# Optimization experiments

Measured on AMD Instinct MI355X. Metric: run time of the kernel, lower is better.

## Reference

```python
import jax, jax.numpy as jnp
import numpy as np

N = 20000      # num nodes
E = 320000     # num edges
F_IN = 512
HEADS = 8
D = 64         # out_features per head (512 / 8)
ALPHA = 0.2    # leaky relu slope
EPS = 1e-16


def setup_inputs() -> dict:
    key = jax.random.key(0)
    k1, k2, k3, k4, k5 = jax.random.split(key, 5)
    x = jax.random.normal(k1, (N, F_IN), dtype=jnp.float32)
    edge_index = jax.random.randint(k2, (2, E), 0, N, dtype=jnp.int64)
    # per-head parameters (xavier-normal-ish scale)
    s_w = np.sqrt(2.0 / (F_IN + D))
    W_e = jax.random.normal(k3, (HEADS, F_IN, D), dtype=jnp.float32) * s_w
    W_r = jax.random.normal(k4, (HEADS, F_IN, D), dtype=jnp.float32) * s_w
    # attention vector over concat of [h_src, h_dst, diff, |diff|, prod] -> 5*D
    s_a = np.sqrt(2.0 / (1 + 5 * D))
    a = jax.random.normal(k5, (HEADS, 5 * D), dtype=jnp.float32) * s_a
    return {"x": x, "edge_index": edge_index, "W_e": W_e, "W_r": W_r, "a": a}


def _gat_forward(x, edge_index, W_e, W_r, a):
    src = edge_index[0]  # [E] softmax / output rows
    dst = edge_index[1]  # [E]

    h_e = jnp.einsum('nf,hfd->hnd', x, W_e)  # [H,N,D]
    h_r = jnp.einsum('nf,hfd->hnd', x, W_r)  # [H,N,D]

    a_src, a_dst, a_dif, a_abs, a_prd = jnp.split(a, 5, axis=1)  # each [H,D]

    # node-level dot products for the linear concat parts, then gather
    s_src = jnp.einsum('hnd,hd->hn', h_e, a_src)[:, src]  # [H,E]
    s_dst = jnp.einsum('hnd,hd->hn', h_e, a_dst)[:, dst]  # [H,E]

    hr_src = h_r[:, src]            # [H,E,D]
    hr_dst = h_r[:, dst]            # [H,E,D]
    diff = hr_dst - hr_src          # [H,E,D]
    score = (s_src + s_dst
             + jnp.einsum('hed,hd->he', diff, a_dif)
             + jnp.einsum('hed,hd->he', jnp.abs(diff), a_abs)
             + jnp.einsum('hed,hd->he', hr_src * hr_dst, a_prd))  # [H,E]

    alpha = jax.nn.leaky_relu(score, negative_slope=ALPHA)  # [H,E]

    # sparse softmax over edges grouped by source node
    alpha_t = alpha.T  # [E,H]
    m = jax.ops.segment_max(alpha_t, src, num_segments=N)        # [N,H]
    ex = jnp.exp(alpha_t - m[src])                                # [E,H]
    denom = jax.ops.segment_sum(ex, src, num_segments=N)[src]    # [E,H]
    att = ex / (denom + EPS)                                      # [E,H]

    # spmm: out[src] += att * h_e[dst]
    msg = att[:, :, None] * jnp.transpose(h_e[:, dst], (1, 0, 2))  # [E,H,D]
    out = jax.ops.segment_sum(msg, src, num_segments=N)            # [N,H,D]
    return out.reshape(N, HEADS * D)  # concat heads along feature dim


def reference(x, edge_index, W_e, W_r, a):
    return _gat_forward(x, edge_index, W_e, W_r, a)
```

## Files before the change

### kernel.cpp

```cpp
#include <hip/hip_runtime.h>
#include <hip/hip_bf16.h>

#define N_NODES 20000
#define N_EDGES 320000
#define F_IN 512
#define HEADS 8
#define DH 64

typedef __attribute__((ext_vector_type(8))) short short8;
typedef __attribute__((ext_vector_type(4))) float f32x4;

__device__ inline short f2bf(float f) {
  __hip_bfloat16 h = __float2bfloat16(f);
  return __builtin_bit_cast(short, h);
}
__device__ inline void unpack8(short8 s, float f[8]) {
  uint4 u = __builtin_bit_cast(uint4, s);
  f[0] = __builtin_bit_cast(float, u.x << 16);
  f[1] = __builtin_bit_cast(float, u.x & 0xFFFF0000u);
  f[2] = __builtin_bit_cast(float, u.y << 16);
  f[3] = __builtin_bit_cast(float, u.y & 0xFFFF0000u);
  f[4] = __builtin_bit_cast(float, u.z << 16);
  f[5] = __builtin_bit_cast(float, u.z & 0xFFFF0000u);
  f[6] = __builtin_bit_cast(float, u.w << 16);
  f[7] = __builtin_bit_cast(float, u.w & 0xFFFF0000u);
}
__device__ __forceinline__ void async_copy16(void* lds_base, const void* g) {
  __builtin_amdgcn_global_load_lds(
      (const __attribute__((address_space(1))) unsigned int*)g,
      (__attribute__((address_space(3))) unsigned int*)lds_base, 16, 0, 0);
}

__global__ __launch_bounds__(256) void cast_x_kernel(
    const float* __restrict__ x, short* __restrict__ xb)
{
  int i = (blockIdx.x * 256 + threadIdx.x) * 4;
  if (i < N_NODES * F_IN) {
    float4 v = *(const float4*)&x[i];
    short4 o;
    o.x = f2bf(v.x); o.y = f2bf(v.y); o.z = f2bf(v.z); o.w = f2bf(v.w);
    *(short4*)&xb[i] = o;
  }
}

__global__ __launch_bounds__(256) void cast_w_kernel(
    const float* __restrict__ We, const float* __restrict__ Wr, short* __restrict__ Wt)
{
  __shared__ short tile[64 * 65];
  const int b = blockIdx.x;
  const int kt = (b & 7) * 64;
  const int h = (b >> 3) & 7;
  const int mat = b >> 6;
  const float* __restrict__ W = (mat ? Wr : We) + (size_t)h * F_IN * DH;
  #pragma unroll
  for (int r = 0; r < 16; ++r) {
    int idx = r * 256 + threadIdx.x;
    int k = idx >> 6, d = idx & 63;
    tile[d * 65 + k] = f2bf(W[(size_t)(kt + k) * DH + d]);
  }
  __syncthreads();
  short* __restrict__ Wo = Wt + (size_t)(mat * 8 + h) * 64 * F_IN;
  #pragma unroll
  for (int r = 0; r < 16; ++r) {
    int idx = r * 256 + threadIdx.x;
    int d = idx >> 6, k = idx & 63;
    Wo[(size_t)d * F_IN + kt + k] = tile[d * 65 + k];
  }
}

#define GBM 128
#define GBN 128
#define GBK 64

__global__ __launch_bounds__(256) void gemm_mfma(
    const short* __restrict__ xb, const short* __restrict__ Wt,
    short* __restrict__ he, short* __restrict__ hr,
    const float* __restrict__ a,
    float* __restrict__ ssrc, float* __restrict__ sdst)
{
  __shared__ short As[GBM * GBK];
  __shared__ short Bs[GBN * GBK];
  const int tid = threadIdx.x;
  const int m0 = blockIdx.x * GBM;
  const int n0 = blockIdx.y * GBN;
  const int wv = tid >> 6, lane = tid & 63, quad = lane >> 4, l16 = lane & 15;
  const int wm = (wv >> 1) * 64;
  const int wn = (wv & 1) * 64;
  const int lrow = lane >> 3;
  const int gc = (lane & 7) ^ (lrow & 7);

  f32x4 acc[4][4] = {};

  for (int kt = 0; kt < F_IN; kt += GBK) {
    #pragma unroll
    for (int s = 0; s < 4; ++s) {
      int seg = wv * 4 + s;
      int row = seg * 8 + lrow;
      async_copy16(&As[seg * 512],
                   &xb[(size_t)(m0 + row) * F_IN + kt + gc * 8]);
      async_copy16(&Bs[seg * 512],
                   &Wt[(size_t)(n0 + row) * F_IN + kt + gc * 8]);
    }
    __syncthreads();
    #pragma unroll
    for (int ks = 0; ks < 2; ++ks) {
      short8 af[4], bf4[4];
      const int ch = ((ks << 2) + quad) ^ (l16 & 7);
      #pragma unroll
      for (int i = 0; i < 4; ++i)
        af[i] = *(const short8*)&As[(wm + i * 16 + l16) * GBK + ch * 8];
      #pragma unroll
      for (int j = 0; j < 4; ++j)
        bf4[j] = *(const short8*)&Bs[(wn + j * 16 + l16) * GBK + ch * 8];
      #pragma unroll
      for (int i = 0; i < 4; ++i)
        #pragma unroll
        for (int j = 0; j < 4; ++j)
          acc[i][j] = __builtin_amdgcn_mfma_f32_16x16x32_bf16(af[i], bf4[j], acc[i][j], 0, 0, 0);
    }
    __syncthreads();
  }

  const int cb = blockIdx.y * 2 + (wv & 1);
  const int mat = cb >> 3, h = cb & 7;
  short* __restrict__ C = mat ? hr : he;
  #pragma unroll
  for (int i = 0; i < 4; ++i) {
    #pragma unroll
    for (int r = 0; r < 4; ++r) {
      int m = m0 + wm + i * 16 + quad * 4 + r;
      if (m < N_NODES) {
        #pragma unroll
        for (int j = 0; j < 4; ++j)
          C[((size_t)m * HEADS + h) * DH + j * 16 + l16] = f2bf(acc[i][j][r]);
      }
    }
  }

  if (mat == 0) {
    float as4[4], ad4[4];
    #pragma unroll
    for (int j = 0; j < 4; ++j) {
      as4[j] = a[h * 320 + j * 16 + l16];
      ad4[j] = a[h * 320 + 64 + j * 16 + l16];
    }
    #pragma unroll
    for (int i = 0; i < 4; ++i) {
      #pragma unroll
      for (int r = 0; r < 4; ++r) {
        int m = m0 + wm + i * 16 + quad * 4 + r;
        float v1 = 0.f, v2 = 0.f;
        #pragma unroll
        for (int j = 0; j < 4; ++j) {
          v1 = fmaf(acc[i][j][r], as4[j], v1);
          v2 = fmaf(acc[i][j][r], ad4[j], v2);
        }
        #pragma unroll
        for (int s = 1; s < 16; s <<= 1) {
          v1 += __shfl_xor(v1, s);
          v2 += __shfl_xor(v2, s);
        }
        if (l16 == 0 && m < N_NODES) {
          ssrc[(size_t)m * HEADS + h] = v1;
          sdst[(size_t)m * HEADS + h] = v2;
        }
      }
    }
  }
}

__global__ void hist_kernel(const int* __restrict__ ei, int* __restrict__ deg) {
  int e = blockIdx.x * blockDim.x + threadIdx.x;
  if (e < N_EDGES) atomicAdd(&deg[ei[e]], 1);
}

#define SC_NB 20

__global__ __launch_bounds__(1024) void scan_pre(
    const int* __restrict__ deg, int* __restrict__ bsum)
{
  __shared__ int wsum[16];
  int tid = threadIdx.x, wv = tid >> 6, ln = tid & 63;
  int i = blockIdx.x * 1024 + tid;
  int v = (i < N_NODES) ? deg[i] : 0;
  #pragma unroll
  for (int d = 32; d >= 1; d >>= 1) v += __shfl_xor(v, d);
  if (ln == 0) wsum[wv] = v;
  __syncthreads();
  if (tid == 0) {
    int s = 0;
    #pragma unroll
    for (int k = 0; k < 16; ++k) s += wsum[k];
    bsum[blockIdx.x] = s;
  }
}

__global__ void scan_mid(const int* __restrict__ bsum, int* __restrict__ bbase,
                         int* __restrict__ off)
{
  int ln = threadIdx.x;
  int v = (ln < SC_NB) ? bsum[ln] : 0;
  int s = v;
  #pragma unroll
  for (int d = 1; d < 64; d <<= 1) {
    int t = __shfl_up(s, d);
    if (ln >= d) s += t;
  }
  if (ln < SC_NB) bbase[ln] = s - v;
  if (ln == SC_NB - 1) off[N_NODES] = s;
}

__global__ __launch_bounds__(1024) void scan_fin(
    const int* __restrict__ deg, const int* __restrict__ bbase, int* __restrict__ off)
{
  __shared__ int wsum[16];
  int tid = threadIdx.x, wv = tid >> 6, ln = tid & 63;
  int i = blockIdx.x * 1024 + tid;
  int v = (i < N_NODES) ? deg[i] : 0;
  int s = v;
  #pragma unroll
  for (int d = 1; d < 64; d <<= 1) {
    int t = __shfl_up(s, d);
    if (ln >= d) s += t;
  }
  if (ln == 63) wsum[wv] = s;
  __syncthreads();
  if (wv == 0 && ln < 16) {
    int t = wsum[ln];
    #pragma unroll
    for (int d = 1; d < 16; d <<= 1) {
      int u = __shfl_up(t, d);
      if (ln >= d) t += u;
    }
    wsum[ln] = t;
  }
  __syncthreads();
  int base = bbase[blockIdx.x] + (wv ? wsum[wv - 1] : 0);
  if (i < N_NODES) off[i] = base + s - v;
}

__global__ void scatter_kernel(const int* __restrict__ ei, const int* __restrict__ off,
                               int* __restrict__ cnt, int* __restrict__ csr_dst) {
  int e = blockIdx.x * blockDim.x + threadIdx.x;
  if (e < N_EDGES) {
    int s = ei[e];
    int t = ei[N_EDGES + e];
    int pos = off[s] + atomicAdd(&cnt[s], 1);
    csr_dst[pos] = t;
  }
}

#define ATTN_BLOCKS 1024
#define ATTN_WAVES (ATTN_BLOCKS * 8)

__global__ __launch_bounds__(512) void attn_kernel(
    const short* __restrict__ he, const short* __restrict__ hr,
    const float* __restrict__ a, const float* __restrict__ ssrc,
    const float* __restrict__ sdst, const int* __restrict__ off,
    const int* __restrict__ csr_dst, float* __restrict__ out)
{
  const int lane = threadIdx.x & 63;
  const int h = lane >> 3;
  const int d0 = (lane & 7) * 8;
  const int ab = h * 320;
  float adif[8], aabs[8], aprd[8];
  *(float4*)&adif[0] = *(const float4*)&a[ab + 128 + d0];
  *(float4*)&adif[4] = *(const float4*)&a[ab + 128 + d0 + 4];
  *(float4*)&aabs[0] = *(const float4*)&a[ab + 192 + d0];
  *(float4*)&aabs[4] = *(const float4*)&a[ab + 192 + d0 + 4];
  *(float4*)&aprd[0] = *(const float4*)&a[ab + 256 + d0];
  *(float4*)&aprd[4] = *(const float4*)&a[ab + 256 + d0 + 4];

  const int gw0 = blockIdx.x * 8 + (threadIdx.x >> 6);

  for (int n = gw0; n < N_NODES; n += ATTN_WAVES) {
    const int beg = off[n], end = off[n + 1];
    float hrn[8];
    unpack8(*(const short8*)&hr[(size_t)n * 512 + lane * 8], hrn);
    const float sbase = ssrc[(size_t)n * HEADS + h];
    float denom = 0.f;
    float acc[8] = {};

    auto edge = [&](short8 hr8, short8 he8, float sd) {
      float hrd[8], hed[8];
      unpack8(hr8, hrd);
      unpack8(he8, hed);
      float v = 0.f;
      #pragma unroll
      for (int j = 0; j < 8; ++j) {
        float df = hrd[j] - hrn[j];
        v = fmaf(df, adif[j], v);
        v = fmaf(fabsf(df), aabs[j], v);
        v = fmaf(hrn[j] * hrd[j], aprd[j], v);
      }
      v += __shfl_xor(v, 1);
      v += __shfl_xor(v, 2);
      v += __shfl_xor(v, 4);
      float sc = sbase + sd + v;
      sc = fmaxf(sc, 0.2f * sc);
      float ex = __expf(sc);
      denom += ex;
      #pragma unroll
      for (int j = 0; j < 8; ++j) acc[j] = fmaf(ex, hed[j], acc[j]);
    };

    int i = beg;
    for (; i + 4 <= end; i += 4) {
      int t0 = csr_dst[i], t1 = csr_dst[i + 1], t2 = csr_dst[i + 2], t3 = csr_dst[i + 3];
      short8 r0 = *(const short8*)&hr[(size_t)t0 * 512 + lane * 8];
      short8 e0 = *(const short8*)&he[(size_t)t0 * 512 + lane * 8];
      short8 r1 = *(const short8*)&hr[(size_t)t1 * 512 + lane * 8];
      short8 e1 = *(const short8*)&he[(size_t)t1 * 512 + lane * 8];
      short8 r2 = *(const short8*)&hr[(size_t)t2 * 512 + lane * 8];
      short8 e2 = *(const short8*)&he[(size_t)t2 * 512 + lane * 8];
      short8 r3 = *(const short8*)&hr[(size_t)t3 * 512 + lane * 8];
      short8 e3 = *(const short8*)&he[(size_t)t3 * 512 + lane * 8];
      float s0 = sdst[(size_t)t0 * HEADS + h];
      float s1 = sdst[(size_t)t1 * HEADS + h];
      float s2 = sdst[(size_t)t2 * HEADS + h];
      float s3 = sdst[(size_t)t3 * HEADS + h];
      edge(r0, e0, s0);
      edge(r1, e1, s1);
      edge(r2, e2, s2);
      edge(r3, e3, s3);
    }
    for (; i < end; ++i) {
      int t = csr_dst[i];
      short8 r0 = *(const short8*)&hr[(size_t)t * 512 + lane * 8];
      short8 e0 = *(const short8*)&he[(size_t)t * 512 + lane * 8];
      float s0 = sdst[(size_t)t * HEADS + h];
      edge(r0, e0, s0);
    }

    float inv = 1.f / (denom + 1e-16f);
    float4 o0, o1;
    o0.x = acc[0] * inv; o0.y = acc[1] * inv; o0.z = acc[2] * inv; o0.w = acc[3] * inv;
    o1.x = acc[4] * inv; o1.y = acc[5] * inv; o1.z = acc[6] * inv; o1.w = acc[7] * inv;
    *(float4*)&out[(size_t)n * 512 + lane * 8] = o0;
    *(float4*)&out[(size_t)n * 512 + lane * 8 + 4] = o1;
  }
}

extern "C" void kernel_launch(void* const* d_in, const int* in_sizes, int n_in,
                              void* d_out, int out_size, void* d_ws, size_t ws_size,
                              hipStream_t stream) {
  const float* x  = (const float*)d_in[0];
  const int*   ei = (const int*)d_in[1];
  const float* We = (const float*)d_in[2];
  const float* Wr = (const float*)d_in[3];
  const float* a  = (const float*)d_in[4];
  float* out = (float*)d_out;

  char* ws = (char*)d_ws;
  size_t p = 0;
  auto alloc = [&](size_t bytes) {
    void* r = ws + p;
    p = (p + bytes + 255) & ~(size_t)255;
    return r;
  };
  short* xb = (short*)alloc(sizeof(short) * (size_t)N_NODES * F_IN);
  short* Wt = (short*)alloc(sizeof(short) * 2 * HEADS * F_IN * DH);
  short* he = (short*)alloc(sizeof(short) * (size_t)N_NODES * HEADS * DH);
  short* hr = (short*)alloc(sizeof(short) * (size_t)N_NODES * HEADS * DH);
  float* ssrc = (float*)alloc(sizeof(float) * (size_t)N_NODES * HEADS);
  float* sdst = (float*)alloc(sizeof(float) * (size_t)N_NODES * HEADS);
  int* degcnt = (int*)alloc(sizeof(int) * 2 * N_NODES);
  int* deg = degcnt;
  int* cnt = degcnt + N_NODES;
  int* off = (int*)alloc(sizeof(int) * (N_NODES + 1));
  int* csr = (int*)alloc(sizeof(int) * N_EDGES);
  int* bsum = (int*)alloc(sizeof(int) * SC_NB);
  int* bbase = (int*)alloc(sizeof(int) * SC_NB);

  hipMemsetAsync(degcnt, 0, sizeof(int) * 2 * N_NODES, stream);

  cast_x_kernel<<<(N_NODES * F_IN / 4 + 255) / 256, 256, 0, stream>>>(x, xb);
  cast_w_kernel<<<128, 256, 0, stream>>>(We, Wr, Wt);

  dim3 g1((N_NODES + GBM - 1) / GBM, 8);
  gemm_mfma<<<g1, 256, 0, stream>>>(xb, Wt, he, hr, a, ssrc, sdst);

  hist_kernel<<<(N_EDGES + 255) / 256, 256, 0, stream>>>(ei, deg);
  scan_pre<<<SC_NB, 1024, 0, stream>>>(deg, bsum);
  scan_mid<<<1, 64, 0, stream>>>(bsum, bbase, off);
  scan_fin<<<SC_NB, 1024, 0, stream>>>(deg, bbase, off);
  scatter_kernel<<<(N_EDGES + 255) / 256, 256, 0, stream>>>(ei, off, cnt, csr);
  attn_kernel<<<ATTN_BLOCKS, 512, 0, stream>>>(he, hr, a, ssrc, sdst, off, csr, out);
}
```

Measured before the change: 281.0 us.

## Remap GEMM blocks per XCD and launch one wave per node in attention

Result: faster. 274.4 us (-2.3%).

```diff
diff --git a/kernel.cpp b/kernel.cpp
--- a/kernel.cpp
+++ b/kernel.cpp
@@ -71,6 +71,8 @@
 #define GBM 128
 #define GBN 128
 #define GBK 64
+#define MT_TOTAL 157
+#define MT_PER_GRP 20
 
 __global__ __launch_bounds__(256) void gemm_mfma(
     const short* __restrict__ xb, const short* __restrict__ Wt,
@@ -78,11 +80,18 @@
     const float* __restrict__ a,
     float* __restrict__ ssrc, float* __restrict__ sdst)
 {
+  const int b = blockIdx.x;
+  const int g = b & 7;
+  const int j = b >> 3;
+  const int m_tile = g * MT_PER_GRP + (j >> 3);
+  const int c_tile = j & 7;
+  if (m_tile >= MT_TOTAL) return;
+
   __shared__ short As[GBM * GBK];
   __shared__ short Bs[GBN * GBK];
   const int tid = threadIdx.x;
-  const int m0 = blockIdx.x * GBM;
-  const int n0 = blockIdx.y * GBN;
+  const int m0 = m_tile * GBM;
+  const int n0 = c_tile * GBN;
   const int wv = tid >> 6, lane = tid & 63, quad = lane >> 4, l16 = lane & 15;
   const int wm = (wv >> 1) * 64;
   const int wn = (wv & 1) * 64;
@@ -110,18 +119,18 @@
       for (int i = 0; i < 4; ++i)
         af[i] = *(const short8*)&As[(wm + i * 16 + l16) * GBK + ch * 8];
       #pragma unroll
-      for (int j = 0; j < 4; ++j)
-        bf4[j] = *(const short8*)&Bs[(wn + j * 16 + l16) * GBK + ch * 8];
+      for (int jj = 0; jj < 4; ++jj)
+        bf4[jj] = *(const short8*)&Bs[(wn + jj * 16 + l16) * GBK + ch * 8];
       #pragma unroll
       for (int i = 0; i < 4; ++i)
         #pragma unroll
-        for (int j = 0; j < 4; ++j)
-          acc[i][j] = __builtin_amdgcn_mfma_f32_16x16x32_bf16(af[i], bf4[j], acc[i][j], 0, 0, 0);
+        for (int jj = 0; jj < 4; ++jj)
+          acc[i][jj] = __builtin_amdgcn_mfma_f32_16x16x32_bf16(af[i], bf4[jj], acc[i][jj], 0, 0, 0);
     }
     __syncthreads();
   }
 
-  const int cb = blockIdx.y * 2 + (wv & 1);
+  const int cb = c_tile * 2 + (wv & 1);
   const int mat = cb >> 3, h = cb & 7;
   short* __restrict__ C = mat ? hr : he;
   #pragma unroll
@@ -131,8 +140,8 @@
       int m = m0 + wm + i * 16 + quad * 4 + r;
       if (m < N_NODES) {
         #pragma unroll
-        for (int j = 0; j < 4; ++j)
-          C[((size_t)m * HEADS + h) * DH + j * 16 + l16] = f2bf(acc[i][j][r]);
+        for (int jj = 0; jj < 4; ++jj)
+          C[((size_t)m * HEADS + h) * DH + jj * 16 + l16] = f2bf(acc[i][jj][r]);
       }
     }
   }
@@ -140,9 +149,9 @@
   if (mat == 0) {
     float as4[4], ad4[4];
     #pragma unroll
-    for (int j = 0; j < 4; ++j) {
-      as4[j] = a[h * 320 + j * 16 + l16];
-      ad4[j] = a[h * 320 + 64 + j * 16 + l16];
+    for (int jj = 0; jj < 4; ++jj) {
+      as4[jj] = a[h * 320 + jj * 16 + l16];
+      ad4[jj] = a[h * 320 + 64 + jj * 16 + l16];
     }
     #pragma unroll
     for (int i = 0; i < 4; ++i) {
@@ -151,9 +160,9 @@
         int m = m0 + wm + i * 16 + quad * 4 + r;
         float v1 = 0.f, v2 = 0.f;
         #pragma unroll
-        for (int j = 0; j < 4; ++j) {
-          v1 = fmaf(acc[i][j][r], as4[j], v1);
-          v2 = fmaf(acc[i][j][r], ad4[j], v2);
+        for (int jj = 0; jj < 4; ++jj) {
+          v1 = fmaf(acc[i][jj][r], as4[jj], v1);
+          v2 = fmaf(acc[i][jj][r], ad4[jj], v2);
         }
         #pragma unroll
         for (int s = 1; s < 16; s <<= 1) {
@@ -250,95 +259,74 @@
   }
 }
 
-#define ATTN_BLOCKS 1024
-#define ATTN_WAVES (ATTN_BLOCKS * 8)
-
-__global__ __launch_bounds__(512) void attn_kernel(
+__global__ __launch_bounds__(256) void attn_kernel(
     const short* __restrict__ he, const short* __restrict__ hr,
     const float* __restrict__ a, const float* __restrict__ ssrc,
     const float* __restrict__ sdst, const int* __restrict__ off,
     const int* __restrict__ csr_dst, float* __restrict__ out)
 {
+  const int wv = threadIdx.x >> 6;
+  const int n = blockIdx.x * 4 + wv;
   const int lane = threadIdx.x & 63;
   const int h = lane >> 3;
   const int d0 = (lane & 7) * 8;
+  const int beg = off[n], end = off[n + 1];
+
+  float hrn[8];
+  unpack8(*(const short8*)&hr[(size_t)n * 512 + lane * 8], hrn);
+  float adif[8], aabs[8], aprd[8];
   const int ab = h * 320;
-  float adif[8], aabs[8], aprd[8];
   *(float4*)&adif[0] = *(const float4*)&a[ab + 128 + d0];
   *(float4*)&adif[4] = *(const float4*)&a[ab + 128 + d0 + 4];
   *(float4*)&aabs[0] = *(const float4*)&a[ab + 192 + d0];
   *(float4*)&aabs[4] = *(const float4*)&a[ab + 192 + d0 + 4];
   *(float4*)&aprd[0] = *(const float4*)&a[ab + 256 + d0];
   *(float4*)&aprd[4] = *(const float4*)&a[ab + 256 + d0 + 4];
-
-  const int gw0 = blockIdx.x * 8 + (threadIdx.x >> 6);
-
-  for (int n = gw0; n < N_NODES; n += ATTN_WAVES) {
-    const int beg = off[n], end = off[n + 1];
-    float hrn[8];
-    unpack8(*(const short8*)&hr[(size_t)n * 512 + lane * 8], hrn);
-    const float sbase = ssrc[(size_t)n * HEADS + h];
-    float denom = 0.f;
-    float acc[8] = {};
-
-    auto edge = [&](short8 hr8, short8 he8, float sd) {
-      float hrd[8], hed[8];
-      unpack8(hr8, hrd);
-      unpack8(he8, hed);
-      float v = 0.f;
-      #pragma unroll
-      for (int j = 0; j < 8; ++j) {
-        float df = hrd[j] - hrn[j];
-        v = fmaf(df, adif[j], v);
-        v = fmaf(fabsf(df), aabs[j], v);
-        v = fmaf(hrn[j] * hrd[j], aprd[j], v);
-      }
-      v += __shfl_xor(v, 1);
-      v += __shfl_xor(v, 2);
-      v += __shfl_xor(v, 4);
-      float sc = sbase + sd + v;
-      sc = fmaxf(sc, 0.2f * sc);
-      float ex = __expf(sc);
-      denom += ex;
-      #pragma unroll
-      for (int j = 0; j < 8; ++j) acc[j] = fmaf(ex, hed[j], acc[j]);
-    };
-
-    int i = beg;
-    for (; i + 4 <= end; i += 4) {
-      int t0 = csr_dst[i], t1 = csr_dst[i + 1], t2 = csr_dst[i + 2], t3 = csr_dst[i + 3];
-      short8 r0 = *(const short8*)&hr[(size_t)t0 * 512 + lane * 8];
-      short8 e0 = *(const short8*)&he[(size_t)t0 * 512 + lane * 8];
-      short8 r1 = *(const short8*)&hr[(size_t)t1 * 512 + lane * 8];
-      short8 e1 = *(const short8*)&he[(size_t)t1 * 512 + lane * 8];
-      short8 r2 = *(const short8*)&hr[(size_t)t2 * 512 + lane * 8];
-      short8 e2 = *(const short8*)&he[(size_t)t2 * 512 + lane * 8];
-      short8 r3 = *(const short8*)&hr[(size_t)t3 * 512 + lane * 8];
-      short8 e3 = *(const short8*)&he[(size_t)t3 * 512 + lane * 8];
-      float s0 = sdst[(size_t)t0 * HEADS + h];
-      float s1 = sdst[(size_t)t1 * HEADS + h];
-      float s2 = sdst[(size_t)t2 * HEADS + h];
-      float s3 = sdst[(size_t)t3 * HEADS + h];
-      edge(r0, e0, s0);
-      edge(r1, e1, s1);
-      edge(r2, e2, s2);
-      edge(r3, e3, s3);
-    }
-    for (; i < end; ++i) {
-      int t = csr_dst[i];
-      short8 r0 = *(const short8*)&hr[(size_t)t * 512 + lane * 8];
-      short8 e0 = *(const short8*)&he[(size_t)t * 512 + lane * 8];
-      float s0 = sdst[(size_t)t * HEADS + h];
-      edge(r0, e0, s0);
-    }
-
-    float inv = 1.f / (denom + 1e-16f);
-    float4 o0, o1;
-    o0.x = acc[0] * inv; o0.y = acc[1] * inv; o0.z = acc[2] * inv; o0.w = acc[3] * inv;
-    o1.x = acc[4] * inv; o1.y = acc[5] * inv; o1.z = acc[6] * inv; o1.w = acc[7] * inv;
-    *(float4*)&out[(size_t)n * 512 + lane * 8] = o0;
-    *(float4*)&out[(size_t)n * 512 + lane * 8 + 4] = o1;
-  }
+  const float sbase = ssrc[(size_t)n * HEADS + h];
+
+  float denom = 0.f;
+  float acc[8] = {};
+
+  auto process = [&](int t) {
+    short8 hr8 = *(const short8*)&hr[(size_t)t * 512 + lane * 8];
+    short8 he8 = *(const short8*)&he[(size_t)t * 512 + lane * 8];
+    float sd = sdst[(size_t)t * HEADS + h];
+    float hrd[8], hed[8];
+    unpack8(hr8, hrd);
+    unpack8(he8, hed);
+    float v = 0.f;
+    #pragma unroll
+    for (int j = 0; j < 8; ++j) {
+      float df = hrd[j] - hrn[j];
+      v = fmaf(df, adif[j], v);
+      v = fmaf(fabsf(df), aabs[j], v);
+      v = fmaf(hrn[j] * hrd[j], aprd[j], v);
+    }
+    v += __shfl_xor(v, 1);
+    v += __shfl_xor(v, 2);
+    v += __shfl_xor(v, 4);
+    float sc = sbase + sd + v;
+    sc = fmaxf(sc, 0.2f * sc);
+    float ex = __expf(sc);
+    denom += ex;
+    #pragma unroll
+    for (int j = 0; j < 8; ++j) acc[j] = fmaf(ex, hed[j], acc[j]);
+  };
+
+  int i = beg;
+  for (; i + 1 < end; i += 2) {
+    int t0 = csr_dst[i], t1 = csr_dst[i + 1];
+    process(t0);
+    process(t1);
+  }
+  if (i < end) process(csr_dst[i]);
+
+  float inv = 1.f / (denom + 1e-16f);
+  float4 o0, o1;
+  o0.x = acc[0] * inv; o0.y = acc[1] * inv; o0.z = acc[2] * inv; o0.w = acc[3] * inv;
+  o1.x = acc[4] * inv; o1.y = acc[5] * inv; o1.z = acc[6] * inv; o1.w = acc[7] * inv;
+  *(float4*)&out[(size_t)n * 512 + lane * 8] = o0;
+  *(float4*)&out[(size_t)n * 512 + lane * 8 + 4] = o1;
 }
 
 extern "C" void kernel_launch(void* const* d_in, const int* in_sizes, int n_in,
@@ -377,13 +365,12 @@
   cast_x_kernel<<<(N_NODES * F_IN / 4 + 255) / 256, 256, 0, stream>>>(x, xb);
   cast_w_kernel<<<128, 256, 0, stream>>>(We, Wr, Wt);
 
-  dim3 g1((N_NODES + GBM - 1) / GBM, 8);
-  gemm_mfma<<<g1, 256, 0, stream>>>(xb, Wt, he, hr, a, ssrc, sdst);
+  gemm_mfma<<<8 * MT_PER_GRP * 8, 256, 0, stream>>>(xb, Wt, he, hr, a, ssrc, sdst);
 
   hist_kernel<<<(N_EDGES + 255) / 256, 256, 0, stream>>>(ei, deg);
   scan_pre<<<SC_NB, 1024, 0, stream>>>(deg, bsum);
   scan_mid<<<1, 64, 0, stream>>>(bsum, bbase, off);
   scan_fin<<<SC_NB, 1024, 0, stream>>>(deg, bbase, off);
   scatter_kernel<<<(N_EDGES + 255) / 256, 256, 0, stream>>>(ei, off, cnt, csr);
-  attn_kernel<<<ATTN_BLOCKS, 512, 0, stream>>>(he, hr, a, ssrc, sdst, off, csr, out);
-}
+  attn_kernel<<<N_NODES / 4, 256, 0, stream>>>(he, hr, a, ssrc, sdst, off, csr, out);
+}
```
